# Optimization experiments

Measured on AMD Instinct MI355X. Metric: run time of the kernel, lower is better.

Reference implementation:

```python
import jax, jax.numpy as jnp
import numpy as np

B, N, D, K = 8, 4096, 1024, 128
LN_EPS = 1e-5


def _layer_norm(x, g, b):
    m = jnp.mean(x, axis=-1, keepdims=True)
    v = jnp.mean(jnp.square(x - m), axis=-1, keepdims=True)
    return (x - m) * jax.lax.rsqrt(v + LN_EPS) * g + b


def setup_inputs() -> dict:
    key = jax.random.key(0)
    ks = jax.random.split(key, 8)
    # conv init in torch: normal(0, sqrt(2 / (k * out_channels))), k=1
    s_dd = np.sqrt(2.0 / D)  # conv_in, conv_out: out_channels = D
    s_kd = np.sqrt(2.0 / K)  # linear_0: out_channels = K
    s_dk = np.sqrt(2.0 / D)  # linear_1: out_channels = D
    return {
        "x": jax.random.normal(ks[0], (B, N, D), dtype=jnp.float32),
        "ln_g": jnp.ones((D,), jnp.float32),
        "ln_b": jnp.zeros((D,), jnp.float32),
        "w_in": jax.random.normal(ks[1], (D, D), jnp.float32) * s_dd,  # (out, in)
        "b_in": jnp.zeros((D,), jnp.float32),
        "w0": jax.random.normal(ks[2], (K, D), jnp.float32) * s_kd,    # linear_0 (K, D)
        "w1": jax.random.normal(ks[3], (D, K), jnp.float32) * s_dk,    # linear_1 (D, K)
        "w_out": jax.random.normal(ks[4], (D, D), jnp.float32) * s_dd,
        "oln_g": jnp.ones((D,), jnp.float32),
        "oln_b": jnp.zeros((D,), jnp.float32),
    }


def reference(x, ln_g, ln_b, w_in, b_in, w0, w1, w_out, oln_g, oln_b):
    idn = x
    h = _layer_norm(x, ln_g, ln_b)                       # (B, N, D)
    h = jnp.einsum("bnd,ed->bne", h, w_in) + b_in        # conv_in 1x1
    a = jnp.einsum("bnd,kd->bnk", h, w0)                 # (B, N, K)
    a = jax.nn.softmax(a, axis=1)                        # softmax over positions N
    a = a / (1e-9 + jnp.sum(a, axis=2, keepdims=True))   # L1 norm over slots K
    h = jnp.einsum("bnk,dk->bnd", a, w1)                 # linear_1
    h = jnp.einsum("bnd,ed->bne", h, w_out)              # conv_out
    h = _layer_norm(h, oln_g, oln_b)
    return jax.nn.relu(h + idn)
```

## Files before the change

kernel.cpp:

```cpp
#include <hip/hip_runtime.h>
#include <hip/hip_bf16.h>
#include <cstdint>
#include <cstddef>

#define BATCH 8
#define SEQN 4096
#define DIM 1024
#define KSLOT 128
#define MROWS (BATCH * SEQN)
#define LN_EPS 1e-5f

typedef __hip_bfloat16 bf16;
typedef __attribute__((ext_vector_type(8))) short short8;
typedef __attribute__((ext_vector_type(4))) float f32x4;

__device__ __forceinline__ float bf2f(unsigned short u) {
    return __uint_as_float(((unsigned int)u) << 16);
}
__device__ __forceinline__ unsigned short f2bf(float f) {
    unsigned int u = __float_as_uint(f);
    unsigned int r = (u + 0x7fffu + ((u >> 16) & 1u)) >> 16;
    return (unsigned short)r;
}
__device__ __forceinline__ float waveReduceSum(float v) {
    #pragma unroll
    for (int off = 32; off > 0; off >>= 1) v += __shfl_down(v, off, 64);
    return v;
}
__device__ __forceinline__ void load4(const float* p, float* o) {
    float4 v = *reinterpret_cast<const float4*>(p);
    o[0] = v.x; o[1] = v.y; o[2] = v.z; o[3] = v.w;
}
__device__ __forceinline__ void store4(float* p, const float* o) {
    float4 v; v.x = o[0]; v.y = o[1]; v.z = o[2]; v.w = o[3];
    *reinterpret_cast<float4*>(p) = v;
}
__device__ __forceinline__ void store4(bf16* p, const float* o) {
    ushort4 v; v.x = f2bf(o[0]); v.y = f2bf(o[1]); v.z = f2bf(o[2]); v.w = f2bf(o[3]);
    *reinterpret_cast<ushort4*>(p) = v;
}

typedef __attribute__((address_space(1))) const void gvoid;
typedef __attribute__((address_space(3))) void lvoid;
__device__ __forceinline__ void async_cp16(const void* g, void* l) {
    __builtin_amdgcn_global_load_lds((gvoid*)g, (lvoid*)l, 16, 0, 0);
}

__global__ __launch_bounds__(256) void nn_partial(
    const float* __restrict__ A, const float* __restrict__ B,
    float* __restrict__ P, int Ka, int E, int Db)
{
    __shared__ float As[16][68];
    __shared__ float Bs[16][68];
    int tid = threadIdx.x, tx = tid & 15, ty = tid >> 4;
    int k0 = blockIdx.x * 64, d0 = blockIdx.y * 64;
    int chunk = E >> 2, e0 = blockIdx.z * chunk;
    int lr = tid >> 2, lk = (tid & 3) * 4;
    int er = tid >> 4, dc = (tid & 15) * 4;
    float acc[4][4] = {};
    for (int et = 0; et < chunk; et += 16) {
        float av[4], bv[4];
        load4(A + (size_t)(k0 + lr) * E + e0 + et + lk, av);
        load4(B + (size_t)(e0 + et + er) * Db + d0 + dc, bv);
        #pragma unroll
        for (int j = 0; j < 4; j++) { As[lk + j][lr] = av[j]; Bs[er][dc + j] = bv[j]; }
        __syncthreads();
        #pragma unroll
        for (int kk = 0; kk < 16; kk++) {
            float a_[4], b_[4];
            #pragma unroll
            for (int i = 0; i < 4; i++) { a_[i] = As[kk][ty * 4 + i]; b_[i] = Bs[kk][tx * 4 + i]; }
            #pragma unroll
            for (int i = 0; i < 4; i++)
                #pragma unroll
                for (int j = 0; j < 4; j++) acc[i][j] += a_[i] * b_[j];
        }
        __syncthreads();
    }
    float* base = P + ((size_t)blockIdx.z * Ka + k0) * Db + d0;
    #pragma unroll
    for (int i = 0; i < 4; i++) store4(base + (size_t)(ty * 4 + i) * Db + tx * 4, acc[i]);
}

__global__ __launch_bounds__(256) void reduce_split(
    const float* __restrict__ P, bf16* __restrict__ hi, bf16* __restrict__ lo, int n)
{
    int i = (blockIdx.x * 256 + threadIdx.x) * 4;
    if (i >= n) return;
    float s0[4], s1[4], s2[4], s3[4];
    load4(P + i, s0);
    load4(P + (size_t)n + i, s1);
    load4(P + 2 * (size_t)n + i, s2);
    load4(P + 3 * (size_t)n + i, s3);
    ushort4 h, l;
    unsigned short hb[4], lb[4];
    #pragma unroll
    for (int j = 0; j < 4; j++) {
        float s = (s0[j] + s1[j]) + (s2[j] + s3[j]);
        hb[j] = f2bf(s);
        lb[j] = f2bf(s - bf2f(hb[j]));
    }
    h.x = hb[0]; h.y = hb[1]; h.z = hb[2]; h.w = hb[3];
    l.x = lb[0]; l.y = lb[1]; l.z = lb[2]; l.w = lb[3];
    reinterpret_cast<ushort4*>(hi)[i >> 2] = h;
    reinterpret_cast<ushort4*>(lo)[i >> 2] = l;
}

__global__ __launch_bounds__(64) void bias_comb(
    const float* __restrict__ w0, const float* __restrict__ b_in, float* __restrict__ bias0)
{
    int k = blockIdx.x, lane = threadIdx.x;
    float s = 0.0f;
    for (int e = lane; e < DIM; e += 64) s += w0[(size_t)k * DIM + e] * b_in[e];
    s = waveReduceSum(s);
    if (lane == 0) bias0[k] = s;
}

__global__ __launch_bounds__(256) void ln_in_kernel(
    const float* __restrict__ x, const float* __restrict__ g,
    const float* __restrict__ b, bf16* __restrict__ out)
{
    int r = blockIdx.x;
    int t = threadIdx.x;
    float v[4];
    load4(x + (size_t)r * DIM + t * 4, v);
    float sum = v[0] + v[1] + v[2] + v[3];
    float sq  = v[0]*v[0] + v[1]*v[1] + v[2]*v[2] + v[3]*v[3];
    sum = waveReduceSum(sum);
    sq  = waveReduceSum(sq);
    __shared__ float sA[4], sB[4];
    __shared__ float mean_s, rstd_s;
    int w = t >> 6;
    if ((t & 63) == 0) { sA[w] = sum; sB[w] = sq; }
    __syncthreads();
    if (t == 0) {
        float S = sA[0] + sA[1] + sA[2] + sA[3];
        float Q = sB[0] + sB[1] + sB[2] + sB[3];
        float mean = S * (1.0f / DIM);
        float var = Q * (1.0f / DIM) - mean * mean;
        mean_s = mean;
        rstd_s = rsqrtf(fmaxf(var, 0.0f) + LN_EPS);
    }
    __syncthreads();
    float mean = mean_s, rstd = rstd_s;
    float gv[4], bv[4], o[4];
    load4(g + t * 4, gv);
    load4(b + t * 4, bv);
    #pragma unroll
    for (int j = 0; j < 4; j++) o[j] = (v[j] - mean) * rstd * gv[j] + bv[j];
    store4(out + (size_t)r * DIM + t * 4, o);
}

template <bool HAS_BIAS>
__global__ __launch_bounds__(256) void gemm_splitB(
    const bf16* __restrict__ A, const bf16* __restrict__ Whi, const bf16* __restrict__ Wlo,
    const float* __restrict__ bias, float* __restrict__ C, int M, int Nout, int Kin)
{
    __shared__ short As[4096];
    __shared__ short Wh[4096];
    __shared__ short Wl[4096];
    const int tid = threadIdx.x, wave = tid >> 6, lane = tid & 63;
    const int wm = wave >> 1, wn = wave & 1;
    const int m0 = blockIdx.x * 128, n0 = blockIdx.y * 128;
    const int srow = tid >> 2, scol = (tid & 3) * 8;
    const bf16* aG0 = A   + (size_t)(m0 + srow) * Kin + scol;
    const bf16* aG1 = aG0 + (size_t)64 * Kin;
    const bf16* hG0 = Whi + (size_t)(n0 + srow) * Kin + scol;
    const bf16* hG1 = hG0 + (size_t)64 * Kin;
    const bf16* lG0 = Wlo + (size_t)(n0 + srow) * Kin + scol;
    const bf16* lG1 = lG0 + (size_t)64 * Kin;
    short* aL0 = As + tid * 8;  short* aL1 = As + 2048 + tid * 8;
    short* hL0 = Wh + tid * 8;  short* hL1 = Wh + 2048 + tid * 8;
    short* lL0 = Wl + tid * 8;  short* lL1 = Wl + 2048 + tid * 8;
    const int fr = lane & 15, kb = (lane >> 4) * 8;

    f32x4 acc[4][4];
    #pragma unroll
    for (int i = 0; i < 4; i++)
        #pragma unroll
        for (int j = 0; j < 4; j++) acc[i][j] = 0.0f;

    for (int kt = 0; kt < Kin; kt += 32) {
        async_cp16(aG0 + kt, aL0);
        async_cp16(aG1 + kt, aL1);
        async_cp16(hG0 + kt, hL0);
        async_cp16(hG1 + kt, hL1);
        async_cp16(lG0 + kt, lL0);
        async_cp16(lG1 + kt, lL1);
        __syncthreads();
        short8 af[4], bh[4], bl[4];
        #pragma unroll
        for (int i = 0; i < 4; i++) {
            af[i] = *(const short8*)(As + (wm * 64 + i * 16 + fr) * 32 + kb);
            bh[i] = *(const short8*)(Wh + (wn * 64 + i * 16 + fr) * 32 + kb);
            bl[i] = *(const short8*)(Wl + (wn * 64 + i * 16 + fr) * 32 + kb);
        }
        #pragma unroll
        for (int i = 0; i < 4; i++)
            #pragma unroll
            for (int j = 0; j < 4; j++) {
                acc[i][j] = __builtin_amdgcn_mfma_f32_16x16x32_bf16(af[i], bh[j], acc[i][j], 0, 0, 0);
                acc[i][j] = __builtin_amdgcn_mfma_f32_16x16x32_bf16(af[i], bl[j], acc[i][j], 0, 0, 0);
            }
        __syncthreads();
    }

    const int crow = (lane >> 4) * 4;
    #pragma unroll
    for (int j = 0; j < 4; j++) {
        int col = n0 + wn * 64 + j * 16 + fr;
        float bv = HAS_BIAS ? bias[col] : 0.0f;
        #pragma unroll
        for (int i = 0; i < 4; i++) {
            int rbase = m0 + wm * 64 + i * 16 + crow;
            #pragma unroll
            for (int r = 0; r < 4; r++)
                C[(size_t)(rbase + r) * Nout + col] = acc[i][j][r] + bv;
        }
    }
}

__global__ __launch_bounds__(256) void smax_part_kernel(
    const float* __restrict__ logits, float* __restrict__ pm, float* __restrict__ ps)
{
    int kb = blockIdx.x, nb = blockIdx.y, b = blockIdx.z;
    int tx = threadIdx.x, ty = threadIdx.y;
    int k = kb * 64 + tx;
    const float* base = logits + ((size_t)b * SEQN) * KSLOT + k;
    int n0 = nb * 256 + ty * 64;
    float m = -1e30f, s = 0.0f;
    for (int j = 0; j < 64; j++) {
        float v = base[(size_t)(n0 + j) * KSLOT];
        if (v > m) { s = s * __expf(m - v) + 1.0f; m = v; }
        else       { s += __expf(v - m); }
    }
    __shared__ float lm[4][64], ls[4][64];
    lm[ty][tx] = m; ls[ty][tx] = s;
    __syncthreads();
    if (ty == 0) {
        #pragma unroll
        for (int q = 1; q < 4; q++) {
            float m2 = lm[q][tx], s2 = ls[q][tx];
            float nm = fmaxf(m, m2);
            s = s * __expf(m - nm) + s2 * __expf(m2 - nm);
            m = nm;
        }
        int col = b * KSLOT + k;
        pm[col * 16 + nb] = m;
        ps[col * 16 + nb] = s;
    }
}

__global__ __launch_bounds__(256) void smax_comb_kernel(
    const float* __restrict__ pm, const float* __restrict__ ps,
    float* __restrict__ cm, float* __restrict__ cs)
{
    int c = blockIdx.x * 256 + threadIdx.x;
    float m = -1e30f, s = 0.0f;
    #pragma unroll
    for (int nb = 0; nb < 16; nb++) {
        float m2 = pm[c * 16 + nb], s2 = ps[c * 16 + nb];
        float nm = fmaxf(m, m2);
        s = s * __expf(m - nm) + s2 * __expf(m2 - nm);
        m = nm;
    }
    cm[c] = m;
    cs[c] = s;
}

__global__ __launch_bounds__(128) void l1_kernel(
    const float* __restrict__ logits, const float* __restrict__ cm,
    const float* __restrict__ cs, bf16* __restrict__ aout)
{
    int r = blockIdx.x;
    int b = r >> 12;
    int k = threadIdx.x;
    int col = b * KSLOT + k;
    float e = __expf(logits[(size_t)r * KSLOT + k] - cm[col]) / cs[col];
    float t = waveReduceSum(e);
    __shared__ float sh[2];
    __shared__ float tot_s;
    if ((k & 63) == 0) sh[k >> 6] = t;
    __syncthreads();
    if (k == 0) tot_s = sh[0] + sh[1];
    __syncthreads();
    float o = e / (1e-9f + tot_s);
    ((unsigned short*)aout)[(size_t)r * KSLOT + k] = f2bf(o);
}

__global__ __launch_bounds__(256) void final_kernel(
    float* __restrict__ h, const float* __restrict__ x,
    const float* __restrict__ g, const float* __restrict__ b)
{
    int r = blockIdx.x;
    int t = threadIdx.x;
    float v[4];
    load4(h + (size_t)r * DIM + t * 4, v);
    float sum = v[0] + v[1] + v[2] + v[3];
    float sq  = v[0]*v[0] + v[1]*v[1] + v[2]*v[2] + v[3]*v[3];
    sum = waveReduceSum(sum);
    sq  = waveReduceSum(sq);
    __shared__ float sA[4], sB[4];
    __shared__ float mean_s, rstd_s;
    int w = t >> 6;
    if ((t & 63) == 0) { sA[w] = sum; sB[w] = sq; }
    __syncthreads();
    if (t == 0) {
        float S = sA[0] + sA[1] + sA[2] + sA[3];
        float Q = sB[0] + sB[1] + sB[2] + sB[3];
        float mean = S * (1.0f / DIM);
        float var = Q * (1.0f / DIM) - mean * mean;
        mean_s = mean;
        rstd_s = rsqrtf(fmaxf(var, 0.0f) + LN_EPS);
    }
    __syncthreads();
    float mean = mean_s, rstd = rstd_s;
    float gv[4], bv[4], xv[4], o[4];
    load4(g + t * 4, gv);
    load4(b + t * 4, bv);
    load4(x + (size_t)r * DIM + t * 4, xv);
    #pragma unroll
    for (int j = 0; j < 4; j++) {
        float z = (v[j] - mean) * rstd * gv[j] + bv[j] + xv[j];
        o[j] = fmaxf(z, 0.0f);
    }
    store4(h + (size_t)r * DIM + t * 4, o);
}

extern "C" void kernel_launch(void* const* d_in, const int* in_sizes, int n_in,
                              void* d_out, int out_size, void* d_ws, size_t ws_size,
                              hipStream_t stream)
{
    const float* x     = (const float*)d_in[0];
    const float* ln_g  = (const float*)d_in[1];
    const float* ln_b  = (const float*)d_in[2];
    const float* w_in  = (const float*)d_in[3];
    const float* b_in  = (const float*)d_in[4];
    const float* w0    = (const float*)d_in[5];
    const float* w1    = (const float*)d_in[6];
    const float* w_out = (const float*)d_in[7];
    const float* oln_g = (const float*)d_in[8];
    const float* oln_b = (const float*)d_in[9];
    float* out = (float*)d_out;

    char* ws = (char*)d_ws;
    bf16*  hln    = (bf16*)ws;
    bf16*  a_bf   = (bf16*)ws;
    float* logits = (float*)(ws + 67108864);
    float* P1     = (float*)(ws + 67108864);
    float* P2     = (float*)(ws + 69206016);
    bf16*  wc_hi  = (bf16*)(ws + 83886080);
    bf16*  wc_lo  = (bf16*)(ws + 84148224);
    bf16*  wc2_hi = (bf16*)(ws + 84410368);
    bf16*  wc2_lo = (bf16*)(ws + 84672512);
    float* bias0  = (float*)(ws + 84934656);
    float* pm     = (float*)(ws + 84935168);
    float* psum   = (float*)(ws + 85000704);
    float* cm     = (float*)(ws + 85066240);
    float* cs     = (float*)(ws + 85070336);

    nn_partial<<<dim3(2, 16, 4), dim3(256), 0, stream>>>(w0, w_in, P1, KSLOT, DIM, DIM);
    nn_partial<<<dim3(16, 2, 4), dim3(256), 0, stream>>>(w_out, w1, P2, DIM, DIM, KSLOT);
    reduce_split<<<dim3(128), dim3(256), 0, stream>>>(P1, wc_hi, wc_lo, KSLOT * DIM);
    reduce_split<<<dim3(128), dim3(256), 0, stream>>>(P2, wc2_hi, wc2_lo, DIM * KSLOT);
    bias_comb<<<dim3(KSLOT), dim3(64), 0, stream>>>(w0, b_in, bias0);
    ln_in_kernel<<<dim3(MROWS), dim3(256), 0, stream>>>(x, ln_g, ln_b, hln);
    gemm_splitB<true><<<dim3(MROWS / 128, KSLOT / 128), dim3(256), 0, stream>>>(
        hln, wc_hi, wc_lo, bias0, logits, MROWS, KSLOT, DIM);
    smax_part_kernel<<<dim3(KSLOT / 64, 16, BATCH), dim3(64, 4), 0, stream>>>(logits, pm, psum);
    smax_comb_kernel<<<dim3(4), dim3(256), 0, stream>>>(pm, psum, cm, cs);
    l1_kernel<<<dim3(MROWS), dim3(128), 0, stream>>>(logits, cm, cs, a_bf);
    gemm_splitB<false><<<dim3(MROWS / 128, DIM / 128), dim3(256), 0, stream>>>(
        a_bf, wc2_hi, wc2_lo, nullptr, out, MROWS, DIM, KSLOT);
    final_kernel<<<dim3(MROWS), dim3(256), 0, stream>>>(out, x, oln_g, oln_b);
}
```

Before: 468.1 us.

## Store conv_out result as bf16, retile logits GEMM, merge weight-fold reductions

The M x D intermediate from the second GEMM is now written as bf16 into a separate workspace buffer and read back by the final LayerNorm kernel, which writes the output. This halves the traffic for that large intermediate. The logits GEMM gets its own 64-row tile kernel so it launches more blocks across the narrow 128-wide output. The weight-folding precompute also moves to an 8-way split with a single merged reduce launch. Rounding the pre-LayerNorm activations to bf16 costs some precision.

```diff
diff --git a/kernel.cpp b/kernel.cpp
--- a/kernel.cpp
+++ b/kernel.cpp
@@ -31,6 +31,10 @@
     float4 v = *reinterpret_cast<const float4*>(p);
     o[0] = v.x; o[1] = v.y; o[2] = v.z; o[3] = v.w;
 }
+__device__ __forceinline__ void load4(const bf16* p, float* o) {
+    ushort4 v = *reinterpret_cast<const ushort4*>(p);
+    o[0] = bf2f(v.x); o[1] = bf2f(v.y); o[2] = bf2f(v.z); o[3] = bf2f(v.w);
+}
 __device__ __forceinline__ void store4(float* p, const float* o) {
     float4 v; v.x = o[0]; v.y = o[1]; v.z = o[2]; v.w = o[3];
     *reinterpret_cast<float4*>(p) = v;
@@ -54,7 +58,7 @@
     __shared__ float Bs[16][68];
     int tid = threadIdx.x, tx = tid & 15, ty = tid >> 4;
     int k0 = blockIdx.x * 64, d0 = blockIdx.y * 64;
-    int chunk = E >> 2, e0 = blockIdx.z * chunk;
+    int chunk = E >> 3, e0 = blockIdx.z * chunk;
     int lr = tid >> 2, lk = (tid & 3) * 4;
     int er = tid >> 4, dc = (tid & 15) * 4;
     float acc[4][4] = {};
@@ -82,23 +86,31 @@
     for (int i = 0; i < 4; i++) store4(base + (size_t)(ty * 4 + i) * Db + tx * 4, acc[i]);
 }
 
-__global__ __launch_bounds__(256) void reduce_split(
-    const float* __restrict__ P, bf16* __restrict__ hi, bf16* __restrict__ lo, int n)
-{
-    int i = (blockIdx.x * 256 + threadIdx.x) * 4;
+__global__ __launch_bounds__(256) void reduce_split8(
+    const float* __restrict__ P1, const float* __restrict__ P2,
+    bf16* __restrict__ hi1, bf16* __restrict__ lo1,
+    bf16* __restrict__ hi2, bf16* __restrict__ lo2, int n)
+{
+    int bid = blockIdx.x;
+    const float* P; bf16 *hi, *lo; int base;
+    if (bid < 128) { P = P1; hi = hi1; lo = lo1; base = bid; }
+    else           { P = P2; hi = hi2; lo = lo2; base = bid - 128; }
+    int i = (base * 256 + threadIdx.x) * 4;
     if (i >= n) return;
-    float s0[4], s1[4], s2[4], s3[4];
-    load4(P + i, s0);
-    load4(P + (size_t)n + i, s1);
-    load4(P + 2 * (size_t)n + i, s2);
-    load4(P + 3 * (size_t)n + i, s3);
+    float s[4] = {0.f, 0.f, 0.f, 0.f};
+    #pragma unroll
+    for (int z = 0; z < 8; z++) {
+        float t[4];
+        load4(P + (size_t)z * n + i, t);
+        #pragma unroll
+        for (int j = 0; j < 4; j++) s[j] += t[j];
+    }
     ushort4 h, l;
     unsigned short hb[4], lb[4];
     #pragma unroll
     for (int j = 0; j < 4; j++) {
-        float s = (s0[j] + s1[j]) + (s2[j] + s3[j]);
-        hb[j] = f2bf(s);
-        lb[j] = f2bf(s - bf2f(hb[j]));
+        hb[j] = f2bf(s[j]);
+        lb[j] = f2bf(s[j] - bf2f(hb[j]));
     }
     h.x = hb[0]; h.y = hb[1]; h.z = hb[2]; h.w = hb[3];
     l.x = lb[0]; l.y = lb[1]; l.z = lb[2]; l.w = lb[3];
@@ -151,10 +163,77 @@
     store4(out + (size_t)r * DIM + t * 4, o);
 }
 
-template <bool HAS_BIAS>
-__global__ __launch_bounds__(256) void gemm_splitB(
+__global__ __launch_bounds__(256) void gemm_logits(
     const bf16* __restrict__ A, const bf16* __restrict__ Whi, const bf16* __restrict__ Wlo,
-    const float* __restrict__ bias, float* __restrict__ C, int M, int Nout, int Kin)
+    const float* __restrict__ bias, float* __restrict__ C, int M, int Kin)
+{
+    __shared__ short As[64 * 32];
+    __shared__ short Wh[128 * 32];
+    __shared__ short Wl[128 * 32];
+    const int tid = threadIdx.x, wave = tid >> 6, lane = tid & 63;
+    const int wm = wave >> 1, wn = wave & 1;
+    const int m0 = blockIdx.x * 64;
+    const int srow = tid >> 2, scol = (tid & 3) * 8;
+    const bf16* aG  = A   + (size_t)(m0 + srow) * Kin + scol;
+    const bf16* hG0 = Whi + (size_t)srow * Kin + scol;
+    const bf16* hG1 = hG0 + (size_t)64 * Kin;
+    const bf16* lG0 = Wlo + (size_t)srow * Kin + scol;
+    const bf16* lG1 = lG0 + (size_t)64 * Kin;
+    short* aL  = As + tid * 8;
+    short* hL0 = Wh + tid * 8;  short* hL1 = Wh + 2048 + tid * 8;
+    short* lL0 = Wl + tid * 8;  short* lL1 = Wl + 2048 + tid * 8;
+    const int fr = lane & 15, kb = (lane >> 4) * 8;
+
+    f32x4 acc[2][4];
+    #pragma unroll
+    for (int i = 0; i < 2; i++)
+        #pragma unroll
+        for (int j = 0; j < 4; j++) acc[i][j] = 0.0f;
+
+    for (int kt = 0; kt < Kin; kt += 32) {
+        async_cp16(aG + kt, aL);
+        async_cp16(hG0 + kt, hL0);
+        async_cp16(hG1 + kt, hL1);
+        async_cp16(lG0 + kt, lL0);
+        async_cp16(lG1 + kt, lL1);
+        __syncthreads();
+        short8 af[2], bh[4], bl[4];
+        #pragma unroll
+        for (int i = 0; i < 2; i++)
+            af[i] = *(const short8*)(As + (wm * 32 + i * 16 + fr) * 32 + kb);
+        #pragma unroll
+        for (int j = 0; j < 4; j++) {
+            bh[j] = *(const short8*)(Wh + (wn * 64 + j * 16 + fr) * 32 + kb);
+            bl[j] = *(const short8*)(Wl + (wn * 64 + j * 16 + fr) * 32 + kb);
+        }
+        #pragma unroll
+        for (int i = 0; i < 2; i++)
+            #pragma unroll
+            for (int j = 0; j < 4; j++) {
+                acc[i][j] = __builtin_amdgcn_mfma_f32_16x16x32_bf16(af[i], bh[j], acc[i][j], 0, 0, 0);
+                acc[i][j] = __builtin_amdgcn_mfma_f32_16x16x32_bf16(af[i], bl[j], acc[i][j], 0, 0, 0);
+            }
+        __syncthreads();
+    }
+
+    const int crow = (lane >> 4) * 4;
+    #pragma unroll
+    for (int j = 0; j < 4; j++) {
+        int col = wn * 64 + j * 16 + fr;
+        float bv = bias[col];
+        #pragma unroll
+        for (int i = 0; i < 2; i++) {
+            int rbase = m0 + wm * 32 + i * 16 + crow;
+            #pragma unroll
+            for (int r = 0; r < 4; r++)
+                C[(size_t)(rbase + r) * KSLOT + col] = acc[i][j][r] + bv;
+        }
+    }
+}
+
+__global__ __launch_bounds__(256) void gemm_h3(
+    const bf16* __restrict__ A, const bf16* __restrict__ Whi, const bf16* __restrict__ Wlo,
+    bf16* __restrict__ C, int M, int Nout, int Kin)
 {
     __shared__ short As[4096];
     __shared__ short Wh[4096];
@@ -209,13 +288,12 @@
     #pragma unroll
     for (int j = 0; j < 4; j++) {
         int col = n0 + wn * 64 + j * 16 + fr;
-        float bv = HAS_BIAS ? bias[col] : 0.0f;
         #pragma unroll
         for (int i = 0; i < 4; i++) {
             int rbase = m0 + wm * 64 + i * 16 + crow;
             #pragma unroll
             for (int r = 0; r < 4; r++)
-                C[(size_t)(rbase + r) * Nout + col] = acc[i][j][r] + bv;
+                *(unsigned short*)(C + (size_t)(rbase + r) * Nout + col) = f2bf(acc[i][j][r]);
         }
     }
 }
@@ -289,8 +367,8 @@
 }
 
 __global__ __launch_bounds__(256) void final_kernel(
-    float* __restrict__ h, const float* __restrict__ x,
-    const float* __restrict__ g, const float* __restrict__ b)
+    const bf16* __restrict__ h, const float* __restrict__ x,
+    const float* __restrict__ g, const float* __restrict__ b, float* __restrict__ out)
 {
     int r = blockIdx.x;
     int t = threadIdx.x;
@@ -324,7 +402,7 @@
         float z = (v[j] - mean) * rstd * gv[j] + bv[j] + xv[j];
         o[j] = fmaxf(z, 0.0f);
     }
-    store4(h + (size_t)r * DIM + t * 4, o);
+    store4(out + (size_t)r * DIM + t * 4, o);
 }
 
 extern "C" void kernel_launch(void* const* d_in, const int* in_sizes, int n_in,
@@ -346,9 +424,10 @@
     char* ws = (char*)d_ws;
     bf16*  hln    = (bf16*)ws;
     bf16*  a_bf   = (bf16*)ws;
+    bf16*  h3b    = (bf16*)(ws + 8388608);
     float* logits = (float*)(ws + 67108864);
     float* P1     = (float*)(ws + 67108864);
-    float* P2     = (float*)(ws + 69206016);
+    float* P2     = (float*)(ws + 71303168);
     bf16*  wc_hi  = (bf16*)(ws + 83886080);
     bf16*  wc_lo  = (bf16*)(ws + 84148224);
     bf16*  wc2_hi = (bf16*)(ws + 84410368);
@@ -359,18 +438,17 @@
     float* cm     = (float*)(ws + 85066240);
     float* cs     = (float*)(ws + 85070336);
 
-    nn_partial<<<dim3(2, 16, 4), dim3(256), 0, stream>>>(w0, w_in, P1, KSLOT, DIM, DIM);
-    nn_partial<<<dim3(16, 2, 4), dim3(256), 0, stream>>>(w_out, w1, P2, DIM, DIM, KSLOT);
-    reduce_split<<<dim3(128), dim3(256), 0, stream>>>(P1, wc_hi, wc_lo, KSLOT * DIM);
-    reduce_split<<<dim3(128), dim3(256), 0, stream>>>(P2, wc2_hi, wc2_lo, DIM * KSLOT);
+    nn_partial<<<dim3(2, 16, 8), dim3(256), 0, stream>>>(w0, w_in, P1, KSLOT, DIM, DIM);
+    nn_partial<<<dim3(16, 2, 8), dim3(256), 0, stream>>>(w_out, w1, P2, DIM, DIM, KSLOT);
+    reduce_split8<<<dim3(256), dim3(256), 0, stream>>>(P1, P2, wc_hi, wc_lo, wc2_hi, wc2_lo, KSLOT * DIM);
     bias_comb<<<dim3(KSLOT), dim3(64), 0, stream>>>(w0, b_in, bias0);
     ln_in_kernel<<<dim3(MROWS), dim3(256), 0, stream>>>(x, ln_g, ln_b, hln);
-    gemm_splitB<true><<<dim3(MROWS / 128, KSLOT / 128), dim3(256), 0, stream>>>(
-        hln, wc_hi, wc_lo, bias0, logits, MROWS, KSLOT, DIM);
+    gemm_logits<<<dim3(MROWS / 64), dim3(256), 0, stream>>>(
+        hln, wc_hi, wc_lo, bias0, logits, MROWS, DIM);
     smax_part_kernel<<<dim3(KSLOT / 64, 16, BATCH), dim3(64, 4), 0, stream>>>(logits, pm, psum);
     smax_comb_kernel<<<dim3(4), dim3(256), 0, stream>>>(pm, psum, cm, cs);
     l1_kernel<<<dim3(MROWS), dim3(128), 0, stream>>>(logits, cm, cs, a_bf);
-    gemm_splitB<false><<<dim3(MROWS / 128, DIM / 128), dim3(256), 0, stream>>>(
-        a_bf, wc2_hi, wc2_lo, nullptr, out, MROWS, DIM, KSLOT);
-    final_kernel<<<dim3(MROWS), dim3(256), 0, stream>>>(out, x, oln_g, oln_b);
-}
+    gemm_h3<<<dim3(MROWS / 128, DIM / 128), dim3(256), 0, stream>>>(
+        a_bf, wc2_hi, wc2_lo, h3b, MROWS, DIM, KSLOT);
+    final_kernel<<<dim3(MROWS), dim3(256), 0, stream>>>(h3b, x, oln_g, oln_b, out);
+}
```

Measured after the change: 412.3 us. 11.9% less time.
